# Optimization experiments

Hardware: AMD Instinct MI355X
Metric: run time of the kernel (lower is better)

Reference implementation:

```python
import jax, jax.numpy as jnp
import numpy as np

N, E, F, L, G, C = 100000, 1600000, 128, 3, 512, 40
BN_EPS = 1e-5


def gcn_conv(x, src, dst, W, b, n_nodes):
    # PyG GCNConv: linear transform, symmetric normalization with self-loops,
    # scatter-add aggregation, then bias.
    xw = x @ W                                   # [N, H]
    deg = jnp.zeros((n_nodes,), x.dtype).at[dst].add(1.0) + 1.0  # +1 self-loop
    dinv = jax.lax.rsqrt(deg)                    # D^{-1/2}
    norm = dinv[src] * dinv[dst]                 # [E]
    msg = xw[src] * norm[:, None]                # gather + scale, [E, H]
    agg = jnp.zeros_like(xw).at[dst].add(msg)    # scatter-add to destinations
    agg = agg + xw * (dinv * dinv)[:, None]      # self-loop contribution
    return agg + b


def setup_inputs() -> dict:
    key = jax.random.key(0)
    ks = jax.random.split(key, 6)
    x = jax.random.normal(ks[0], (N, F), dtype=jnp.float32)
    edge_index = jax.random.randint(ks[1], (2, E), 0, N, dtype=jnp.int64)
    batch = jnp.sort(jax.random.randint(ks[2], (N,), 0, G, dtype=jnp.int64))
    conv_w = jax.random.normal(ks[3], (L, F, F), dtype=jnp.float32) * 0.05
    conv_b = jnp.zeros((L, F), dtype=jnp.float32)
    bn_gamma = jnp.ones((L, F), dtype=jnp.float32)
    bn_beta = jnp.zeros((L, F), dtype=jnp.float32)
    bn_mean = jnp.zeros((L, F), dtype=jnp.float32)
    bn_var = jnp.ones((L, F), dtype=jnp.float32)
    lin_w = jax.random.normal(ks[4], (F, C), dtype=jnp.float32) * 0.05
    lin_b = jnp.zeros((C,), dtype=jnp.float32)
    return {"x": x, "edge_index": edge_index, "batch": batch,
            "conv_w": conv_w, "conv_b": conv_b,
            "bn_gamma": bn_gamma, "bn_beta": bn_beta,
            "bn_mean": bn_mean, "bn_var": bn_var,
            "lin_w": lin_w, "lin_b": lin_b}


def reference(x, edge_index, batch, conv_w, conv_b, bn_gamma, bn_beta,
              bn_mean, bn_var, lin_w, lin_b):
    src, dst = edge_index[0], edge_index[1]
    h = x
    # layers 0..L-2: conv -> BN(eval) -> ReLU (dropout is identity in eval)
    for i in range(L - 1):
        h = gcn_conv(h, src, dst, conv_w[i], conv_b[i], N)
        h = (h - bn_mean[i]) * (bn_gamma[i] * jax.lax.rsqrt(bn_var[i] + BN_EPS)) + bn_beta[i]
        h = jax.nn.relu(h)
    # last conv (no BN/ReLU)
    h = gcn_conv(h, src, dst, conv_w[L - 1], conv_b[L - 1], N)
    # global_mean_pool over graphs
    sums = jnp.zeros((G, F), h.dtype).at[batch].add(h)
    counts = jnp.zeros((G,), h.dtype).at[batch].add(1.0)
    pooled = sums / jnp.maximum(counts, 1.0)[:, None]   # [G, F]
    return pooled @ lin_w + lin_b                        # [G, C]
```

## Files before the change

### kernel.cpp

```cpp
#include <hip/hip_runtime.h>

#define Nn 100000
#define Ee 1600000
#define Ff 128
#define Gg 512
#define Cc 40
#define NCH 2048
#define CH  49

__global__ void prep_scales_k(const float* __restrict__ conv_b,
                              const float* __restrict__ gamma,
                              const float* __restrict__ beta,
                              const float* __restrict__ mean,
                              const float* __restrict__ var,
                              float* __restrict__ sc, float* __restrict__ sh)
{
    int i = blockIdx.x * blockDim.x + threadIdx.x;
    if (i >= 3 * Ff) return;
    float b = conv_b[i];
    if (i < 2 * Ff) {
        float s = gamma[i] * rsqrtf(var[i] + 1e-5f);
        sc[i] = s;
        sh[i] = (b - mean[i]) * s + beta[i];
    } else {
        sc[i] = 1.0f;
        sh[i] = b;
    }
}

__global__ void count_edges_k(const int* __restrict__ dst, int* __restrict__ deg)
{
    int e = blockIdx.x * 256 + threadIdx.x;
    if (e < Ee) atomicAdd(&deg[dst[e]], 1);
}

__global__ void chunk_sum_k(const int* __restrict__ deg, int* __restrict__ csum)
{
    int t = blockIdx.x * 256 + threadIdx.x;
    if (t >= NCH) return;
    int i0 = t * CH, i1 = min(i0 + CH, Nn);
    int s = 0;
    for (int i = i0; i < i1; ++i) s += deg[i];
    csum[t] = s;
}

__global__ void scan_chunks_k(const int* __restrict__ csum, int* __restrict__ coff)
{
    __shared__ int tot[256];
    int t = threadIdx.x;
    int v[8]; int s = 0;
    #pragma unroll
    for (int j = 0; j < 8; ++j) { v[j] = csum[t * 8 + j]; s += v[j]; }
    tot[t] = s;
    __syncthreads();
    for (int d = 1; d < 256; d <<= 1) {
        int x = (t >= d) ? tot[t - d] : 0;
        __syncthreads();
        tot[t] += x;
        __syncthreads();
    }
    int base = tot[t] - s;
    #pragma unroll
    for (int j = 0; j < 8; ++j) { coff[t * 8 + j] = base; base += v[j]; }
}

__global__ void write_offsets_k(const int* __restrict__ deg, const int* __restrict__ coff,
                                int* __restrict__ off, float* __restrict__ dinv)
{
    int t = blockIdx.x * 256 + threadIdx.x;
    if (t >= NCH) return;
    int i0 = t * CH, i1 = min(i0 + CH, Nn);
    int run = coff[t];
    for (int i = i0; i < i1; ++i) {
        off[i] = run;
        int d = deg[i];
        run += d;
        dinv[i] = rsqrtf((float)d + 1.0f);
    }
    if (t == 0) off[Nn] = Ee;
}

__global__ void fill_csr_k(const int* __restrict__ src, const int* __restrict__ dst,
                           const int* __restrict__ off, int* __restrict__ cur,
                           int* __restrict__ csrc)
{
    int e = blockIdx.x * 256 + threadIdx.x;
    if (e < Ee) {
        int d = dst[e];
        int p = off[d] + atomicAdd(&cur[d], 1);
        csrc[p] = src[e];
    }
}

__global__ __launch_bounds__(256) void gemm_scale_k(
    const float* __restrict__ A, const float* __restrict__ W,
    const float* __restrict__ dinv, float* __restrict__ Y, int n)
{
    const int lane = threadIdx.x & 63;
    const int wv   = threadIdx.x >> 6;
    const int colBase = __builtin_amdgcn_readfirstlane(wv) * 32;
    const int r0 = blockIdx.x * 128 + lane;
    const int r1 = r0 + 64;
    const float* a0p = A + (size_t)min(r0, n - 1) * Ff;
    const float* a1p = A + (size_t)min(r1, n - 1) * Ff;
    const float* Wp  = W + colBase;

    float acc0[32], acc1[32];
    #pragma unroll
    for (int c = 0; c < 32; ++c) { acc0[c] = 0.f; acc1[c] = 0.f; }

    #pragma unroll 2
    for (int k4 = 0; k4 < 32; ++k4) {
        const float4 a0 = *(const float4*)(a0p + k4 * 4);
        const float4 a1 = *(const float4*)(a1p + k4 * 4);
        #pragma unroll
        for (int kk = 0; kk < 4; ++kk) {
            const float* wr = Wp + (k4 * 4 + kk) * Ff;
            const float av0 = (&a0.x)[kk];
            const float av1 = (&a1.x)[kk];
            #pragma unroll
            for (int c = 0; c < 32; ++c) {
                const float wvv = wr[c];
                acc0[c] = fmaf(av0, wvv, acc0[c]);
                acc1[c] = fmaf(av1, wvv, acc1[c]);
            }
        }
    }

    if (r0 < n) {
        const float di = dinv[r0];
        float* yp = Y + (size_t)r0 * Ff + colBase;
        #pragma unroll
        for (int c = 0; c < 32; c += 4)
            *(float4*)(yp + c) = make_float4(acc0[c] * di, acc0[c + 1] * di,
                                             acc0[c + 2] * di, acc0[c + 3] * di);
    }
    if (r1 < n) {
        const float di = dinv[r1];
        float* yp = Y + (size_t)r1 * Ff + colBase;
        #pragma unroll
        for (int c = 0; c < 32; c += 4)
            *(float4*)(yp + c) = make_float4(acc1[c] * di, acc1[c + 1] * di,
                                             acc1[c + 2] * di, acc1[c + 3] * di);
    }
}

__global__ __launch_bounds__(256) void aggregate_k(
    const float* __restrict__ Y, const int* __restrict__ off,
    const int* __restrict__ srcs, const float* __restrict__ dinv,
    const float* __restrict__ sc, const float* __restrict__ sh,
    float* __restrict__ H, int dorelu, int n)
{
    const int wid  = threadIdx.x >> 6;
    const int lane = threadIdx.x & 63;
    const int node = blockIdx.x * 4 + wid;
    if (node >= n) return;
    const int beg = off[node], end = off[node + 1];
    const int half = lane >> 5;
    const int fl   = lane & 31;
    const float4* Y4 = (const float4*)Y;

    float ax = 0.f, ay = 0.f, az = 0.f, aw = 0.f;
    float bx = 0.f, by = 0.f, bz = 0.f, bw = 0.f;
    if (half == 0) {
        float4 s4 = Y4[(size_t)node * 32 + fl];
        ax = s4.x; ay = s4.y; az = s4.z; aw = s4.w;
    }

    for (int e = beg; e < end; e += 64) {
        const int nb = min(64, end - e);
        int sidx = (lane < nb) ? srcs[e + lane] : 0;
        int j = 0;
        for (; j + 8 <= nb; j += 8) {
            int s0 = __shfl(sidx, j + 0 + half);
            int s1 = __shfl(sidx, j + 2 + half);
            int s2 = __shfl(sidx, j + 4 + half);
            int s3 = __shfl(sidx, j + 6 + half);
            float4 v0 = Y4[(size_t)s0 * 32 + fl];
            float4 v1 = Y4[(size_t)s1 * 32 + fl];
            float4 v2 = Y4[(size_t)s2 * 32 + fl];
            float4 v3 = Y4[(size_t)s3 * 32 + fl];
            ax += v0.x; ay += v0.y; az += v0.z; aw += v0.w;
            bx += v1.x; by += v1.y; bz += v1.z; bw += v1.w;
            ax += v2.x; ay += v2.y; az += v2.z; aw += v2.w;
            bx += v3.x; by += v3.y; bz += v3.z; bw += v3.w;
        }
        for (; j < nb; j += 2) {
            const int eo = j + half;
            int s = __shfl(sidx, (eo < nb) ? eo : (nb - 1));
            if (eo < nb) {
                float4 v = Y4[(size_t)s * 32 + fl];
                ax += v.x; ay += v.y; az += v.z; aw += v.w;
            }
        }
    }
    ax += bx; ay += by; az += bz; aw += bw;
    float rx = ax + __shfl_xor(ax, 32);
    float ry = ay + __shfl_xor(ay, 32);
    float rz = az + __shfl_xor(az, 32);
    float rw = aw + __shfl_xor(aw, 32);

    if (half == 0) {
        const float di = dinv[node];
        const float4 scv = ((const float4*)sc)[fl];
        const float4 shv = ((const float4*)sh)[fl];
        float4 o;
        o.x = rx * di * scv.x + shv.x;
        o.y = ry * di * scv.y + shv.y;
        o.z = rz * di * scv.z + shv.z;
        o.w = rw * di * scv.w + shv.w;
        if (dorelu) {
            o.x = fmaxf(o.x, 0.f); o.y = fmaxf(o.y, 0.f);
            o.z = fmaxf(o.z, 0.f); o.w = fmaxf(o.w, 0.f);
        }
        ((float4*)H)[(size_t)node * 32 + fl] = o;
    }
}

__global__ __launch_bounds__(128) void pool_linear_k(
    const float* __restrict__ H, const int* __restrict__ batch,
    const float* __restrict__ lw, const float* __restrict__ lb,
    float* __restrict__ out)
{
    int g = blockIdx.x, f = threadIdx.x;
    int lo = 0, hi = Nn;
    while (lo < hi) { int m = (lo + hi) >> 1; if (batch[m] < g) lo = m + 1; else hi = m; }
    int start = lo;
    hi = Nn;
    while (lo < hi) { int m = (lo + hi) >> 1; if (batch[m] < g + 1) lo = m + 1; else hi = m; }
    int end = lo;

    float a0 = 0.f, a1 = 0.f, a2 = 0.f, a3 = 0.f;
    int i = start;
    for (; i + 4 <= end; i += 4) {
        a0 += H[(size_t)(i + 0) * Ff + f];
        a1 += H[(size_t)(i + 1) * Ff + f];
        a2 += H[(size_t)(i + 2) * Ff + f];
        a3 += H[(size_t)(i + 3) * Ff + f];
    }
    for (; i < end; ++i) a0 += H[(size_t)i * Ff + f];
    int cnt = end - start;
    __shared__ float pooled[Ff];
    pooled[f] = ((a0 + a1) + (a2 + a3)) / (float)max(cnt, 1);
    __syncthreads();
    if (f < Cc) {
        float o = lb[f];
        #pragma unroll 8
        for (int k = 0; k < Ff; ++k) o += pooled[k] * lw[k * Cc + f];
        out[g * Cc + f] = o;
    }
}

extern "C" void kernel_launch(void* const* d_in, const int* in_sizes, int n_in,
                              void* d_out, int out_size, void* d_ws, size_t ws_size,
                              hipStream_t stream)
{
    const float* x      = (const float*)d_in[0];
    const int*   ei     = (const int*)d_in[1];
    const int*   batch  = (const int*)d_in[2];
    const float* conv_w = (const float*)d_in[3];
    const float* conv_b = (const float*)d_in[4];
    const float* gamma  = (const float*)d_in[5];
    const float* beta   = (const float*)d_in[6];
    const float* mean   = (const float*)d_in[7];
    const float* var    = (const float*)d_in[8];
    const float* lw     = (const float*)d_in[9];
    const float* lb     = (const float*)d_in[10];
    float* out = (float*)d_out;

    const int* srcp = ei;
    const int* dstp = ei + Ee;

    float* h    = (float*)d_ws;
    float* y    = h + (size_t)Nn * Ff;
    float* dinv = y + (size_t)Nn * Ff;
    float* sc   = dinv + Nn;
    float* sh   = sc + 3 * Ff;
    int*   deg  = (int*)(sh + 3 * Ff);
    int*   cur  = deg + Nn;
    int*   off  = cur + Nn;
    int*   csrc = off + (Nn + 1);
    int*   csum = csrc + Ee;
    int*   coff = csum + NCH;

    hipMemsetAsync(deg, 0, 2 * (size_t)Nn * sizeof(int), stream);

    prep_scales_k<<<2, 256, 0, stream>>>(conv_b, gamma, beta, mean, var, sc, sh);
    count_edges_k<<<Ee / 256, 256, 0, stream>>>(dstp, deg);
    chunk_sum_k<<<NCH / 256, 256, 0, stream>>>(deg, csum);
    scan_chunks_k<<<1, 256, 0, stream>>>(csum, coff);
    write_offsets_k<<<NCH / 256, 256, 0, stream>>>(deg, coff, off, dinv);
    fill_csr_k<<<Ee / 256, 256, 0, stream>>>(srcp, dstp, off, cur, csrc);

    const int gemm_grid = (Nn + 127) / 128;
    const int agg_grid  = (Nn + 3) / 4;
    for (int l = 0; l < 3; ++l) {
        const float* in = (l == 0) ? x : h;
        gemm_scale_k<<<gemm_grid, 256, 0, stream>>>(in, conv_w + (size_t)l * Ff * Ff,
                                                    dinv, y, Nn);
        aggregate_k<<<agg_grid, 256, 0, stream>>>(y, off, csrc, dinv,
                                                  sc + l * Ff, sh + l * Ff,
                                                  h, (l < 2) ? 1 : 0, Nn);
    }
    pool_linear_k<<<Gg, 128, 0, stream>>>(h, batch, lw, lb, out);
}
```

Baseline: 858.7 us.

## Split aggregation into feature halves, fuse mean-pool into last layer, retile GEMM

Aggregation now runs twice per layer, each pass covering 64 feature columns, so the working set of gathered rows is half as large and may fit better in cache. Each lane now loads one scalar per neighbour instead of a float4. The final layer's aggregation adds its output into per-graph pool sums with atomics, so the last H write and the separate pooling read are gone. The GEMM switches to one row per thread with 64 accumulator columns. The risks are lower memory-level parallelism from scalar gathers, twice as many passes over the CSR index lists, atomic contention on the pool sums, and register pressure from the 64 accumulators.

```diff
diff --git a/kernel.cpp b/kernel.cpp
--- a/kernel.cpp
+++ b/kernel.cpp
@@ -96,129 +96,104 @@
     const float* __restrict__ A, const float* __restrict__ W,
     const float* __restrict__ dinv, float* __restrict__ Y, int n)
 {
-    const int lane = threadIdx.x & 63;
-    const int wv   = threadIdx.x >> 6;
-    const int colBase = __builtin_amdgcn_readfirstlane(wv) * 32;
-    const int r0 = blockIdx.x * 128 + lane;
-    const int r1 = r0 + 64;
-    const float* a0p = A + (size_t)min(r0, n - 1) * Ff;
-    const float* a1p = A + (size_t)min(r1, n - 1) * Ff;
-    const float* Wp  = W + colBase;
-
-    float acc0[32], acc1[32];
+    const int tid  = threadIdx.x;
+    const int half = __builtin_amdgcn_readfirstlane(tid >> 7);
+    const int cb   = half * 64;
+    const int r    = blockIdx.x * 128 + (tid & 127);
+    const int rr   = min(r, n - 1);
+    const float4* Ap = (const float4*)(A + ((size_t)rr << 7));
+    const float*  Wp = W + cb;
+
+    float acc[64];
     #pragma unroll
-    for (int c = 0; c < 32; ++c) { acc0[c] = 0.f; acc1[c] = 0.f; }
-
-    #pragma unroll 2
-    for (int k4 = 0; k4 < 32; ++k4) {
-        const float4 a0 = *(const float4*)(a0p + k4 * 4);
-        const float4 a1 = *(const float4*)(a1p + k4 * 4);
+    for (int c = 0; c < 64; ++c) acc[c] = 0.f;
+
+    for (int kc = 0; kc < 4; ++kc) {
+        float4 a[8];
         #pragma unroll
-        for (int kk = 0; kk < 4; ++kk) {
-            const float* wr = Wp + (k4 * 4 + kk) * Ff;
-            const float av0 = (&a0.x)[kk];
-            const float av1 = (&a1.x)[kk];
+        for (int i = 0; i < 8; ++i) a[i] = Ap[kc * 8 + i];
+        const float* af = reinterpret_cast<const float*>(a);
+        #pragma unroll
+        for (int kk = 0; kk < 32; ++kk) {
+            const float av = af[kk];
+            const float* wr = Wp + (kc * 32 + kk) * Ff;
             #pragma unroll
-            for (int c = 0; c < 32; ++c) {
-                const float wvv = wr[c];
-                acc0[c] = fmaf(av0, wvv, acc0[c]);
-                acc1[c] = fmaf(av1, wvv, acc1[c]);
-            }
+            for (int c = 0; c < 64; ++c)
+                acc[c] = fmaf(av, wr[c], acc[c]);
         }
     }
 
-    if (r0 < n) {
-        const float di = dinv[r0];
-        float* yp = Y + (size_t)r0 * Ff + colBase;
+    if (r < n) {
+        const float di = dinv[r];
+        float* yp = Y + ((size_t)r << 7) + cb;
         #pragma unroll
-        for (int c = 0; c < 32; c += 4)
-            *(float4*)(yp + c) = make_float4(acc0[c] * di, acc0[c + 1] * di,
-                                             acc0[c + 2] * di, acc0[c + 3] * di);
-    }
-    if (r1 < n) {
-        const float di = dinv[r1];
-        float* yp = Y + (size_t)r1 * Ff + colBase;
-        #pragma unroll
-        for (int c = 0; c < 32; c += 4)
-            *(float4*)(yp + c) = make_float4(acc1[c] * di, acc1[c + 1] * di,
-                                             acc1[c + 2] * di, acc1[c + 3] * di);
-    }
-}
-
-__global__ __launch_bounds__(256) void aggregate_k(
+        for (int c = 0; c < 64; c += 4)
+            *(float4*)(yp + c) = make_float4(acc[c] * di, acc[c + 1] * di,
+                                             acc[c + 2] * di, acc[c + 3] * di);
+    }
+}
+
+__global__ __launch_bounds__(256) void aggregate_half_k(
     const float* __restrict__ Y, const int* __restrict__ off,
     const int* __restrict__ srcs, const float* __restrict__ dinv,
     const float* __restrict__ sc, const float* __restrict__ sh,
-    float* __restrict__ H, int dorelu, int n)
+    const int* __restrict__ batch,
+    float* __restrict__ H, float* __restrict__ pool,
+    int cb, int dorelu, int n)
 {
     const int wid  = threadIdx.x >> 6;
     const int lane = threadIdx.x & 63;
     const int node = blockIdx.x * 4 + wid;
     if (node >= n) return;
     const int beg = off[node], end = off[node + 1];
-    const int half = lane >> 5;
-    const int fl   = lane & 31;
-    const float4* Y4 = (const float4*)Y;
-
-    float ax = 0.f, ay = 0.f, az = 0.f, aw = 0.f;
-    float bx = 0.f, by = 0.f, bz = 0.f, bw = 0.f;
-    if (half == 0) {
-        float4 s4 = Y4[(size_t)node * 32 + fl];
-        ax = s4.x; ay = s4.y; az = s4.z; aw = s4.w;
-    }
+    const float* Yc = Y + cb + lane;
+
+    float acc  = Yc[node << 7];
+    float acc2 = 0.f;
 
     for (int e = beg; e < end; e += 64) {
         const int nb = min(64, end - e);
         int sidx = (lane < nb) ? srcs[e + lane] : 0;
         int j = 0;
         for (; j + 8 <= nb; j += 8) {
-            int s0 = __shfl(sidx, j + 0 + half);
-            int s1 = __shfl(sidx, j + 2 + half);
-            int s2 = __shfl(sidx, j + 4 + half);
-            int s3 = __shfl(sidx, j + 6 + half);
-            float4 v0 = Y4[(size_t)s0 * 32 + fl];
-            float4 v1 = Y4[(size_t)s1 * 32 + fl];
-            float4 v2 = Y4[(size_t)s2 * 32 + fl];
-            float4 v3 = Y4[(size_t)s3 * 32 + fl];
-            ax += v0.x; ay += v0.y; az += v0.z; aw += v0.w;
-            bx += v1.x; by += v1.y; bz += v1.z; bw += v1.w;
-            ax += v2.x; ay += v2.y; az += v2.z; aw += v2.w;
-            bx += v3.x; by += v3.y; bz += v3.z; bw += v3.w;
+            int s0 = __shfl(sidx, j + 0);
+            int s1 = __shfl(sidx, j + 1);
+            int s2 = __shfl(sidx, j + 2);
+            int s3 = __shfl(sidx, j + 3);
+            int s4 = __shfl(sidx, j + 4);
+            int s5 = __shfl(sidx, j + 5);
+            int s6 = __shfl(sidx, j + 6);
+            int s7 = __shfl(sidx, j + 7);
+            float v0 = Yc[s0 << 7];
+            float v1 = Yc[s1 << 7];
+            float v2 = Yc[s2 << 7];
+            float v3 = Yc[s3 << 7];
+            float v4 = Yc[s4 << 7];
+            float v5 = Yc[s5 << 7];
+            float v6 = Yc[s6 << 7];
+            float v7 = Yc[s7 << 7];
+            acc += v0; acc2 += v1; acc += v2; acc2 += v3;
+            acc += v4; acc2 += v5; acc += v6; acc2 += v7;
         }
-        for (; j < nb; j += 2) {
-            const int eo = j + half;
-            int s = __shfl(sidx, (eo < nb) ? eo : (nb - 1));
-            if (eo < nb) {
-                float4 v = Y4[(size_t)s * 32 + fl];
-                ax += v.x; ay += v.y; az += v.z; aw += v.w;
-            }
+        for (; j < nb; ++j) {
+            int s = __shfl(sidx, j);
+            acc += Yc[s << 7];
         }
     }
-    ax += bx; ay += by; az += bz; aw += bw;
-    float rx = ax + __shfl_xor(ax, 32);
-    float ry = ay + __shfl_xor(ay, 32);
-    float rz = az + __shfl_xor(az, 32);
-    float rw = aw + __shfl_xor(aw, 32);
-
-    if (half == 0) {
-        const float di = dinv[node];
-        const float4 scv = ((const float4*)sc)[fl];
-        const float4 shv = ((const float4*)sh)[fl];
-        float4 o;
-        o.x = rx * di * scv.x + shv.x;
-        o.y = ry * di * scv.y + shv.y;
-        o.z = rz * di * scv.z + shv.z;
-        o.w = rw * di * scv.w + shv.w;
-        if (dorelu) {
-            o.x = fmaxf(o.x, 0.f); o.y = fmaxf(o.y, 0.f);
-            o.z = fmaxf(o.z, 0.f); o.w = fmaxf(o.w, 0.f);
-        }
-        ((float4*)H)[(size_t)node * 32 + fl] = o;
-    }
-}
-
-__global__ __launch_bounds__(128) void pool_linear_k(
-    const float* __restrict__ H, const int* __restrict__ batch,
+    acc += acc2;
+
+    const float di = dinv[node];
+    float o = acc * di * sc[cb + lane] + sh[cb + lane];
+    if (dorelu) o = fmaxf(o, 0.f);
+    if (pool) {
+        atomicAdd(&pool[(batch[node] << 7) + cb + lane], o);
+    } else {
+        H[(node << 7) + cb + lane] = o;
+    }
+}
+
+__global__ __launch_bounds__(128) void out_k(
+    const float* __restrict__ pool, const int* __restrict__ batch,
     const float* __restrict__ lw, const float* __restrict__ lb,
     float* __restrict__ out)
 {
@@ -228,20 +203,11 @@
     int start = lo;
     hi = Nn;
     while (lo < hi) { int m = (lo + hi) >> 1; if (batch[m] < g + 1) lo = m + 1; else hi = m; }
-    int end = lo;
-
-    float a0 = 0.f, a1 = 0.f, a2 = 0.f, a3 = 0.f;
-    int i = start;
-    for (; i + 4 <= end; i += 4) {
-        a0 += H[(size_t)(i + 0) * Ff + f];
-        a1 += H[(size_t)(i + 1) * Ff + f];
-        a2 += H[(size_t)(i + 2) * Ff + f];
-        a3 += H[(size_t)(i + 3) * Ff + f];
-    }
-    for (; i < end; ++i) a0 += H[(size_t)i * Ff + f];
-    int cnt = end - start;
+    int cnt = lo - start;
+    float invc = 1.0f / (float)max(cnt, 1);
+
     __shared__ float pooled[Ff];
-    pooled[f] = ((a0 + a1) + (a2 + a3)) / (float)max(cnt, 1);
+    pooled[f] = pool[(g << 7) + f] * invc;
     __syncthreads();
     if (f < Cc) {
         float o = lb[f];
@@ -278,12 +244,13 @@
     float* sh   = sc + 3 * Ff;
     int*   deg  = (int*)(sh + 3 * Ff);
     int*   cur  = deg + Nn;
-    int*   off  = cur + Nn;
+    float* pool = (float*)(cur + Nn);
+    int*   off  = (int*)(pool + Gg * Ff);
     int*   csrc = off + (Nn + 1);
     int*   csum = csrc + Ee;
     int*   coff = csum + NCH;
 
-    hipMemsetAsync(deg, 0, 2 * (size_t)Nn * sizeof(int), stream);
+    hipMemsetAsync(deg, 0, (2 * (size_t)Nn + Gg * Ff) * sizeof(int), stream);
 
     prep_scales_k<<<2, 256, 0, stream>>>(conv_b, gamma, beta, mean, var, sc, sh);
     count_edges_k<<<Ee / 256, 256, 0, stream>>>(dstp, deg);
@@ -298,9 +265,11 @@
         const float* in = (l == 0) ? x : h;
         gemm_scale_k<<<gemm_grid, 256, 0, stream>>>(in, conv_w + (size_t)l * Ff * Ff,
                                                     dinv, y, Nn);
-        aggregate_k<<<agg_grid, 256, 0, stream>>>(y, off, csrc, dinv,
-                                                  sc + l * Ff, sh + l * Ff,
-                                                  h, (l < 2) ? 1 : 0, Nn);
-    }
-    pool_linear_k<<<Gg, 128, 0, stream>>>(h, batch, lw, lb, out);
-}
+        float* poolp = (l == 2) ? pool : nullptr;
+        for (int p = 0; p < 2; ++p)
+            aggregate_half_k<<<agg_grid, 256, 0, stream>>>(
+                y, off, csrc, dinv, sc + l * Ff, sh + l * Ff, batch,
+                h, poolp, p * 64, (l < 2) ? 1 : 0, Nn);
+    }
+    out_k<<<Gg, 128, 0, stream>>>(pool, batch, lw, lb, out);
+}
```

Result: slower. 912.1 us (+6.2%).
